# Optimization experiments

Measured on AMD Instinct MI355X. Metric: run time of the kernel, lower is better.

## Reference

```python
import jax, jax.numpy as jnp
import numpy as np

N = 50000      # nodes
E = 800000     # edges (avg degree 16)
H = 128        # hidden_dim
F_IN = 128     # node_in_dim
EPS = 1e-8     # torch cosine_similarity eps
ALPHA = 0.3


def _xavier(k, shape):
    fan_out, fan_in = shape
    lim = float(np.sqrt(6.0 / (fan_in + fan_out)))
    return jax.random.uniform(k, shape, minval=-lim, maxval=lim, dtype=jnp.float32)


PARAM_SHAPES = [
    ("w_lq", (H, 1)), ("w_lf", (H, F_IN)),
    ("wq0", (H, 1)), ("wq1", (H, H)), ("wq2", (H, H)),
    ("wx0", (H, F_IN)), ("wx1", (H, H)), ("wx2", (H, H)),
    ("wf0", (H, H)), ("wf1", (H, H)), ("wf2", (H, H)),
    ("m1_w1", (H, H)), ("m1_w2", (H, H)),
    ("m2_w1", (1, H)), ("m2_w2", (1, 1)),
]
BIAS_OF = {"w_lq": "b_lq", "w_lf": "b_lf", "wq0": "bq0", "wq1": "bq1", "wq2": "bq2",
           "wx0": "bx0", "wx1": "bx1", "wx2": "bx2", "wf0": "bf0", "wf1": "bf1",
           "wf2": "bf2", "m1_w1": "m1_b1", "m1_w2": "m1_b2", "m2_w1": "m2_b1", "m2_w2": "m2_b2"}


def setup_inputs() -> dict:
    key = jax.random.key(0)
    ks = jax.random.split(key, 3 + len(PARAM_SHAPES))
    inp = {
        "q": 42,
        "feats": jax.random.normal(ks[0], (N, F_IN), dtype=jnp.float32),
        "edge_index": jax.random.randint(ks[1], (2, E), 0, N, dtype=jnp.int64),
        "neg_edge_index": jax.random.randint(ks[2], (2, E), 0, N, dtype=jnp.int64),
    }
    for i, (name, shape) in enumerate(PARAM_SHAPES):
        inp[name] = _xavier(ks[3 + i], shape)
        inp[BIAS_OF[name]] = jnp.zeros((shape[0],), jnp.float32)
    return inp


def _forward(q, feats, edge_index, neg_edge_index,
             w_lq, b_lq, w_lf, b_lf,
             wq0, bq0, wq1, bq1, wq2, bq2,
             wx0, bx0, wx1, bx1, wx2, bx2,
             wf0, bf0, wf1, bf1, wf2, bf2,
             m1_w1, m1_b1, m1_w2, m1_b2,
             m2_w1, m2_b1, m2_w2, m2_b2):
    n = feats.shape[0]
    src, dst = edge_index[0], edge_index[1]

    # GCN symmetric normalization with self-loops (edge_weight = 1)
    deg = jax.ops.segment_sum(jnp.ones(src.shape[0], feats.dtype), dst, num_segments=n) + 1.0
    dis = deg ** -0.5
    norm_e = dis[src] * dis[dst]        # per-edge norm
    inv_deg = 1.0 / deg                 # self-loop norm d^-1/2 * d^-1/2

    def lin(x, W, b):
        return x @ W.T + b

    def gcn(x, W, b):
        xw = x @ W.T                                                      # [n,H]
        agg = jax.ops.segment_sum(xw[src] * norm_e[:, None], dst, num_segments=n)
        return agg + xw * inv_deg[:, None] + b

    querys = jnp.zeros((n, 1), feats.dtype).at[q, 0].set(1.0)
    querys_ = lin(querys, w_lq, b_lq)
    feats_ = lin(feats, w_lf, b_lf)

    # layer 0
    hq = jax.nn.relu(gcn(querys, wq0, bq0))
    h = jax.nn.relu(gcn(feats, wx0, bx0))
    hf = jax.nn.relu(hq + h + gcn(querys_ + feats_, wf0, bf0))
    # middle layer (num_layers - 2 == 1 iteration, eval mode: dropout identity)
    hq = jax.nn.relu(gcn(hq, wq1, bq1))
    h = jax.nn.relu(gcn(h, wx1, bx1))
    hf = jax.nn.relu(hq + h + gcn(hf, wf1, bf1))
    # final layer (no relu)
    hq = gcn(hq, wq2, bq2)
    h = gcn(h, wx2, bx2)
    hf = hq + h + gcn(hf, wf2, bf2)

    x = lin(jax.nn.relu(lin(hf, m1_w1, m1_b1)), m1_w2, m1_b2)  # mlp1

    # ---- decode (attack_type != 'proposed') ----
    q_emb = x[q]
    qn = jnp.maximum(jnp.linalg.norm(q_emb), EPS)

    def cos_q(v):  # cosine similarity of rows of v with q_emb (torch eps semantics)
        vn = jnp.maximum(jnp.linalg.norm(v, axis=-1), EPS)
        return (v @ q_emb) / (vn * qn)

    # reconstruct loss: BCE-with-logits on cosine edge scores
    pos_s = cos_q((x[src] + x[dst]) * 0.5)
    neg_s = cos_q((x[neg_edge_index[0]] + x[neg_edge_index[1]]) * 0.5)
    loss_recon = jnp.mean(jax.nn.softplus(-pos_s)) + jnp.mean(jax.nn.softplus(neg_s))

    sim_xq = cos_q(x)                                            # [n]
    sim_xx = lin(jax.nn.relu(lin(x, m2_w1, m2_b1)), m2_w2, m2_b2)[:, 0]  # mlp2
    sim = ((1.0 - ALPHA) * sim_xq + ALPHA * sim_xx) * 2.0
    return jax.nn.sigmoid(sim), loss_recon


def reference(q, feats, edge_index, neg_edge_index,
              w_lq, b_lq, w_lf, b_lf,
              wq0, bq0, wq1, bq1, wq2, bq2,
              wx0, bx0, wx1, bx1, wx2, bx2,
              wf0, bf0, wf1, bf1, wf2, bf2,
              m1_w1, m1_b1, m1_w2, m1_b2,
              m2_w1, m2_b1, m2_w2, m2_b2):
    return _forward(q, feats, edge_index, neg_edge_index,
                    w_lq, b_lq, w_lf, b_lf,
                    wq0, bq0, wq1, bq1, wq2, bq2,
                    wx0, bx0, wx1, bx1, wx2, bx2,
                    wf0, bf0, wf1, bf1, wf2, bf2,
                    m1_w1, m1_b1, m1_w2, m1_b2,
                    m2_w1, m2_b1, m2_w2, m2_b2)
```

## Files before the change

kernel.cpp:

```cpp
#include <hip/hip_runtime.h>
#include <math.h>

#define N_NODES 50000
#define N_EDGES 800000
#define EPSV 1e-8f
#define ALPHA 0.3f

typedef __attribute__((ext_vector_type(8))) unsigned short ushort8;
typedef __attribute__((ext_vector_type(4))) float floatx4;
typedef __attribute__((ext_vector_type(2))) long longx2;
typedef _Float16 half8 __attribute__((ext_vector_type(8)));
typedef _Float16 half2v __attribute__((ext_vector_type(2)));

__device__ inline unsigned short f2h(float f) {
    union { _Float16 h; unsigned short u; } c; c.h = (_Float16)f; return c.u;
}
__device__ inline float h2f(unsigned short u) {
    union { unsigned short u; _Float16 h; } c; c.u = u; return (float)c.h;
}
__device__ inline unsigned char f2e4m3(float f) {
    unsigned u = __float_as_uint(f);
    unsigned s = (u >> 24) & 0x80u;
    float af = fabsf(f);
    if (af >= 464.f) return (unsigned char)(s | 0x7Eu);
    if (af < 0.015625f) {
        int m = (int)rintf(af * 512.f);
        return (unsigned char)(s | (unsigned)m);
    }
    unsigned au = __float_as_uint(af);
    unsigned mant = au & 0x7FFFFFu;
    unsigned lsb = (mant >> 20) & 1u;
    mant += 0x7FFFFu + lsb;
    unsigned exp32 = (au >> 23) + (mant >> 23);
    mant &= 0x7FFFFFu;
    unsigned e8 = exp32 - 127u + 7u;
    return (unsigned char)(s | (e8 << 3) | (mant >> 20));
}
__device__ inline int qperm(int k) {
    return ((k >> 3) & 3) * 32 + (k >> 5) * 8 + (k & 7);
}


__global__ __launch_bounds__(256) void k_count(const int* __restrict__ ei,
                                               int* __restrict__ cnt) {
    int e = blockIdx.x * 256 + threadIdx.x;
    if (e < N_EDGES) atomicAdd(&cnt[__builtin_nontemporal_load(ei + N_EDGES + e)], 1);
}

__global__ __launch_bounds__(256) void k_invdis(const int* __restrict__ cnt,
                                                float* __restrict__ dis,
                                                float* __restrict__ inv) {
    int i = blockIdx.x * 256 + threadIdx.x;
    if (i < N_NODES) {
        float d = (float)cnt[i] + 1.0f;
        dis[i] = 1.0f / sqrtf(d);
        inv[i] = 1.0f / d;
    }
}

__global__ __launch_bounds__(256) void k_scan_partial(const int* __restrict__ cnt,
                                                      int* __restrict__ partial) {
    int b = blockIdx.x, t = threadIdx.x;
    int base = b * 1024 + t * 4;
    int s = 0;
#pragma unroll
    for (int j = 0; j < 4; ++j) {
        int idx = base + j;
        if (idx < N_NODES) s += cnt[idx];
    }
#pragma unroll
    for (int m = 1; m < 64; m <<= 1) s += __shfl_xor(s, m, 64);
    __shared__ int sh[4];
    if ((t & 63) == 0) sh[t >> 6] = s;
    __syncthreads();
    if (t == 0) partial[b] = sh[0] + sh[1] + sh[2] + sh[3];
}

__global__ void k_scan_mid(int* __restrict__ partial, int* __restrict__ rowptr) {
    int l = threadIdx.x;
    const int NP = (N_NODES + 1023) / 1024;
    int v = (l < NP) ? partial[l] : 0;
    int vin = v;
#pragma unroll
    for (int off = 1; off < 64; off <<= 1) {
        int u = __shfl_up(v, off, 64);
        if (l >= off) v += u;
    }
    if (l < NP) partial[l] = v - vin;
    if (l == NP - 1) rowptr[N_NODES] = v;
}

__global__ __launch_bounds__(256) void k_scan_final(const int* __restrict__ cnt,
                                                    const int* __restrict__ partial,
                                                    int* __restrict__ rowptr) {
    int b = blockIdx.x, t = threadIdx.x;
    int base = b * 1024 + t * 4;
    int c[4];
    int s = 0;
#pragma unroll
    for (int j = 0; j < 4; ++j) {
        int idx = base + j;
        c[j] = (idx < N_NODES) ? cnt[idx] : 0;
        s += c[j];
    }
    __shared__ int sh[256];
    sh[t] = s;
    __syncthreads();
    for (int off = 1; off < 256; off <<= 1) {
        int v = 0;
        if (t >= off) v = sh[t - off];
        __syncthreads();
        sh[t] += v;
        __syncthreads();
    }
    int texcl = sh[t] - s;
    int pre = partial[b] + texcl;
#pragma unroll
    for (int j = 0; j < 4; ++j) {
        int idx = base + j;
        if (idx < N_NODES) rowptr[idx] = pre;
        pre += c[j];
    }
}

__global__ __launch_bounds__(256) void k_fill(const int* __restrict__ ei,
                                              const int* __restrict__ rowptr,
                                              int* __restrict__ cursor,
                                              int* __restrict__ col) {
    int e = blockIdx.x * 256 + threadIdx.x;
    if (e < N_EDGES) {
        int d = __builtin_nontemporal_load(ei + N_EDGES + e);
        int pos = rowptr[d] + atomicAdd(&cursor[d], 1);
        col[pos] = __builtin_nontemporal_load(ei + e);
    }
}

__global__ __launch_bounds__(256) void k_t(const int* __restrict__ ei,
                                           const int* __restrict__ qp,
                                           const float* __restrict__ dis,
                                           const float* __restrict__ inv,
                                           float* __restrict__ t) {
    int e = blockIdx.x * 256 + threadIdx.x;
    int q = *qp;
    if (e == 0) atomicAdd(&t[q], inv[q]);
    if (e < N_EDGES && __builtin_nontemporal_load(ei + e) == q) {
        int d = ei[N_EDGES + e];
        atomicAdd(&t[d], dis[q] * dis[d]);
    }
}

__global__ void k_rank1(const float* __restrict__ bq0, const float* __restrict__ bq1,
                        const float* __restrict__ wq0, const float* __restrict__ wq1,
                        const float* __restrict__ wq2, int* __restrict__ flag,
                        float* __restrict__ r0v, float* __restrict__ r1v,
                        float* __restrict__ g2v) {
    int j = threadIdx.x;
    unsigned long long b = __ballot(bq0[j] != 0.f || bq1[j] != 0.f);
    __shared__ int bad[2];
    __shared__ float r0s[128], r1s[128];
    if ((j & 63) == 0) bad[j >> 6] = (b != 0ull);
    __syncthreads();
    int fl = !(bad[0] | bad[1]);
    if (j == 0) flag[0] = fl;
    if (!fl) return;
    float r0 = fmaxf(wq0[j], 0.f);
    r0s[j] = r0;
    r0v[j] = r0;
    __syncthreads();
    float s = 0.f;
    for (int k = 0; k < 128; k += 4) {
        float4 w = *(const float4*)(wq1 + j * 128 + k);
        s += w.x * r0s[k] + w.y * r0s[k + 1] + w.z * r0s[k + 2] + w.w * r0s[k + 3];
    }
    float r1 = fmaxf(s, 0.f);
    r1s[j] = r1;
    r1v[j] = r1;
    __syncthreads();
    float s2 = 0.f;
    for (int k = 0; k < 128; k += 4) {
        float4 w = *(const float4*)(wq2 + j * 128 + k);
        s2 += w.x * r1s[k] + w.y * r1s[k + 1] + w.z * r1s[k + 2] + w.w * r1s[k + 3];
    }
    g2v[j] = s2;
}

__global__ __launch_bounds__(256) void k_spmv(const int* __restrict__ gflag,
                                              const int* __restrict__ rowptr,
                                              const int* __restrict__ col,
                                              const float* __restrict__ dis,
                                              const float* __restrict__ inv,
                                              const float* __restrict__ vin,
                                              float* __restrict__ vout) {
    if (*gflag != 1) return;
    int i = blockIdx.x * 256 + threadIdx.x;
    if (i >= N_NODES) return;
    int r0 = rowptr[i], r1 = rowptr[i + 1];
    float s = 0.f;
    for (int e = r0; e < r1; ++e) {
        int c = col[e];
        s += dis[c] * vin[c];
    }
    vout[i] = fmaf(inv[i], vin[i], dis[i] * s);
}

__global__ __launch_bounds__(256) void k_cast(const float* __restrict__ in,
                                              unsigned short* __restrict__ out, int n8) {
    int id = blockIdx.x * 256 + threadIdx.x;
    if (id >= n8) return;
    const float4 a = *(const float4*)(in + id * 8);
    const float4 b = *(const float4*)(in + id * 8 + 4);
    ushort8 o;
    o[0] = f2h(a.x); o[1] = f2h(a.y); o[2] = f2h(a.z); o[3] = f2h(a.w);
    o[4] = f2h(b.x); o[5] = f2h(b.y); o[6] = f2h(b.z); o[7] = f2h(b.w);
    *(ushort8*)(out + id * 8) = o;
}

struct WPack { const float* w[11]; };
__global__ __launch_bounds__(256) void k_castw(WPack wp, unsigned short* __restrict__ out) {
    int m = blockIdx.y;
    int id = blockIdx.x * 256 + threadIdx.x;
    const float* src = wp.w[m] + id * 8;
    float4 a = *(const float4*)src;
    float4 b = *(const float4*)(src + 4);
    ushort8 o;
    o[0] = f2h(a.x); o[1] = f2h(a.y); o[2] = f2h(a.z); o[3] = f2h(a.w);
    o[4] = f2h(b.x); o[5] = f2h(b.y); o[6] = f2h(b.z); o[7] = f2h(b.w);
    *(ushort8*)(out + m * 16384 + id * 8) = o;
}


__device__ __forceinline__ void gemm_core(
    const unsigned short* __restrict__ A, int As,
    const unsigned short* __restrict__ Wb, int nrows, int row0,
    unsigned short* Al, unsigned short* Wl, floatx4 (&acc)[8][2]) {
    const int tid = threadIdx.x;
    const int wv = tid >> 6;
    const int t4 = tid >> 4, c16 = tid & 15;

#pragma unroll
    for (int it = 0; it < 8; ++it) {
        int r = it * 16 + t4;
        int gr = row0 + r; if (gr > nrows - 1) gr = nrows - 1;
        int sw = (c16 * 16) ^ ((r & 7) << 4);
        const char* srcA = (const char*)(A + (size_t)gr * As) + sw;
        __builtin_amdgcn_global_load_lds(
            (const __attribute__((address_space(1))) void*)srcA,
            (__attribute__((address_space(3))) void*)(Al + it * 2048 + wv * 512),
            16, 0, 0);
        const char* srcW = (const char*)(Wb + r * 128) + sw;
        __builtin_amdgcn_global_load_lds(
            (const __attribute__((address_space(1))) void*)srcW,
            (__attribute__((address_space(3))) void*)(Wl + it * 2048 + wv * 512),
            16, 0, 0);
    }
    __syncthreads();

    const int l = tid & 63;
    const int lr = l & 15, lg = l >> 4;
    const int sx = (lr & 7) << 4;

#pragma unroll
    for (int i = 0; i < 8; ++i)
#pragma unroll
        for (int j = 0; j < 2; ++j) acc[i][j] = (floatx4){0.f, 0.f, 0.f, 0.f};

#pragma unroll
    for (int ks = 0; ks < 4; ++ks) {
        int ko = (ks * 64 + lg * 16) ^ sx;
        half8 bfr[2];
#pragma unroll
        for (int ct = 0; ct < 2; ++ct) {
            int c = wv * 32 + ct * 16 + lr;
            bfr[ct] = *(const half8*)((char*)Wl + c * 256 + ko);
        }
#pragma unroll
        for (int rt = 0; rt < 8; ++rt) {
            int r = rt * 16 + lr;
            half8 af = *(const half8*)((char*)Al + r * 256 + ko);
            acc[rt][0] = __builtin_amdgcn_mfma_f32_16x16x32_f16(af, bfr[0], acc[rt][0], 0, 0, 0);
            acc[rt][1] = __builtin_amdgcn_mfma_f32_16x16x32_f16(af, bfr[1], acc[rt][1], 0, 0, 0);
        }
    }
}

template <int RELU, int HASB2, int WOUT>
__global__ __launch_bounds__(256) void k_gemm(
    const unsigned short* __restrict__ A, int As,
    const unsigned short* __restrict__ Wb,
    const float* __restrict__ bias, const float* __restrict__ bias2,
    const int* __restrict__ gflag, int want,
    unsigned short* __restrict__ outh, int ohs,
    float* __restrict__ outf, unsigned char* __restrict__ outq, int nrows) {
    if (gflag && *gflag != want) return;
    __shared__ unsigned short Al[128 * 128];
    __shared__ unsigned short Wl[128 * 128];
    const int row0 = blockIdx.x * 128;
    floatx4 acc[8][2];
    gemm_core(A, As, Wb, nrows, row0, Al, Wl, acc);

    const int l = threadIdx.x & 63, wv = threadIdx.x >> 6;
    const int lr = l & 15, lg = l >> 4;
#pragma unroll
    for (int ct = 0; ct < 2; ++ct) {
        int colc = wv * 32 + ct * 16 + lr;
        float bv = bias[colc];
        if (HASB2) bv += bias2[colc];
        int qp_ = WOUT == 2 ? qperm(colc) : 0;
#pragma unroll
        for (int rt = 0; rt < 8; ++rt) {
            int rbase = row0 + rt * 16 + lg * 4;
#pragma unroll
            for (int reg = 0; reg < 4; ++reg) {
                int r = rbase + reg;
                if (r >= nrows) continue;
                float v = acc[rt][ct][reg] + bv;
                if (RELU) v = fmaxf(v, 0.f);
                if (WOUT == 2) {
                    outf[(size_t)r * 128 + colc] = v;
                    outq[(size_t)r * 128 + qp_] = f2e4m3(v);
                } else {
                    outh[(size_t)r * ohs + colc] = f2h(v);
                }
            }
        }
    }
}

template <int RELU>
__global__ __launch_bounds__(256) void k_gemmF(
    const unsigned short* __restrict__ A, int As,
    const unsigned short* __restrict__ Wb,
    const float* __restrict__ bias, const float* __restrict__ bias2,
    const unsigned short* __restrict__ addh, int ahs,
    const unsigned short* __restrict__ addhq, int aqs,
    const float* __restrict__ u, const float* __restrict__ vq,
    const int* __restrict__ gflag,
    unsigned short* __restrict__ outh, int ohs, int nrows) {
    __shared__ unsigned short Al[128 * 128];
    __shared__ unsigned short Wl[128 * 128];
    const int row0 = blockIdx.x * 128;
    floatx4 acc[8][2];
    gemm_core(A, As, Wb, nrows, row0, Al, Wl, acc);

    const int fl = *gflag;
    const int l = threadIdx.x & 63, wv = threadIdx.x >> 6;
    const int lr = l & 15, lg = l >> 4;
#pragma unroll
    for (int ct = 0; ct < 2; ++ct) {
        int colc = wv * 32 + ct * 16 + lr;
        float bv = bias[colc];
        float vqc = 0.f;
        if (fl) {
            vqc = vq[colc];
            if (bias2) bv += bias2[colc];
        }
#pragma unroll
        for (int rt = 0; rt < 8; ++rt) {
            int rbase = row0 + rt * 16 + lg * 4;
#pragma unroll
            for (int reg = 0; reg < 4; ++reg) {
                int r = rbase + reg;
                if (r >= nrows) continue;
                float v = acc[rt][ct][reg] + bv;
                if (fl) v = fmaf(u[r], vqc, v);
                else v += h2f(addhq[(size_t)r * aqs + colc]);
                v += h2f(addh[(size_t)r * ahs + colc]);
                if (RELU) v = fmaxf(v, 0.f);
                outh[(size_t)r * ohs + colc] = f2h(v);
            }
        }
    }
}


template <int NUM>
__device__ __forceinline__ void agg_body(
    const int* __restrict__ rowptr, const int* __restrict__ col,
    const float* __restrict__ dis, const float* __restrict__ inv,
    const unsigned short* __restrict__ in0, int s0,
    const unsigned short* __restrict__ in1, int s1,
    const unsigned short* __restrict__ in2, int s2,
    unsigned short* __restrict__ out, int o0, int o1, int o2) {
    int i = blockIdx.x * 4 + (threadIdx.x >> 6);
    int l = threadIdx.x & 63;
    int g = l >> 4, li = l & 15;
    int r0 = rowptr[i], r1 = rowptr[i + 1];

    half2v accA[NUM][4], accB[NUM][4];
#pragma unroll
    for (int b = 0; b < NUM; ++b)
#pragma unroll
        for (int j = 0; j < 4; ++j) {
            accA[b][j] = (half2v){(_Float16)0, (_Float16)0};
            accB[b][j] = (half2v){(_Float16)0, (_Float16)0};
        }

    union U8 { ushort8 u; half2v h[4]; };
    const unsigned short* ins[3] = {in0, in1, in2};
    const int ss[3] = {s0, s1, s2};

    for (int base = r0; base < r1; base += 8) {
        int eA = base + g, eB = base + 4 + g;
        int sA = i; float wA = 0.f;
        if (eA < r1) { sA = col[eA]; wA = dis[sA]; }
        int sB = i; float wB = 0.f;
        if (eB < r1) { sB = col[eB]; wB = dis[sB]; }
        _Float16 whA = (_Float16)wA, whB = (_Float16)wB;
        half2v w2A = {whA, whA}, w2B = {whB, whB};
        U8 vA[NUM], vB[NUM];
#pragma unroll
        for (int b = 0; b < NUM; ++b) {
            vA[b].u = *(const ushort8*)(ins[b] + (size_t)sA * ss[b] + li * 8);
            vB[b].u = *(const ushort8*)(ins[b] + (size_t)sB * ss[b] + li * 8);
        }
#pragma unroll
        for (int b = 0; b < NUM; ++b)
#pragma unroll
            for (int j = 0; j < 4; ++j) {
                accA[b][j] += vA[b].h[j] * w2A;
                accB[b][j] += vB[b].h[j] * w2B;
            }
    }
    union U2 { half2v h; int i; };
#pragma unroll
    for (int b = 0; b < NUM; ++b)
#pragma unroll
        for (int j = 0; j < 4; ++j) {
            U2 c, o;
            c.h = accA[b][j] + accB[b][j];
            o.i = __shfl_xor(c.i, 16, 64); c.h += o.h;
            o.i = __shfl_xor(c.i, 32, 64); c.h += o.h;
            accA[b][j] = c.h;
        }
    if (g == 0) {
        float di = dis[i], iv = inv[i];
        const int oo[3] = {o0, o1, o2};
#pragma unroll
        for (int b = 0; b < NUM; ++b) {
            U8 sv;
            sv.u = *(const ushort8*)(ins[b] + (size_t)i * ss[b] + li * 8);
            ushort8 o;
#pragma unroll
            for (int j = 0; j < 4; ++j) {
                float a0 = fmaf(di, (float)accA[b][j][0], iv * (float)sv.h[j][0]);
                float a1 = fmaf(di, (float)accA[b][j][1], iv * (float)sv.h[j][1]);
                o[2 * j] = f2h(a0);
                o[2 * j + 1] = f2h(a1);
            }
            *(ushort8*)(out + (size_t)i * 384 + oo[b] + li * 8) = o;
        }
    }
}

__global__ __launch_bounds__(256) void k_agg0(
    const int* __restrict__ rowptr, const int* __restrict__ col,
    const float* __restrict__ dis, const float* __restrict__ inv,
    const unsigned short* __restrict__ featsh, const unsigned short* __restrict__ z0h,
    unsigned short* __restrict__ out) {
    agg_body<2>(rowptr, col, dis, inv, featsh, 128, z0h, 128, nullptr, 0,
                out, 128, 256, 0);
}

__global__ __launch_bounds__(256) void k_aggL(
    const int* __restrict__ gflag,
    const int* __restrict__ rowptr, const int* __restrict__ col,
    const float* __restrict__ dis, const float* __restrict__ inv,
    const unsigned short* __restrict__ B1h, unsigned short* __restrict__ B2h) {
    if (*gflag == 1)
        agg_body<2>(rowptr, col, dis, inv, B1h + 128, 384, B1h + 256, 384,
                    nullptr, 0, B2h, 128, 256, 0);
    else
        agg_body<3>(rowptr, col, dis, inv, B1h, 384, B1h + 128, 384,
                    B1h + 256, 384, B2h, 0, 128, 256);
}

__global__ __launch_bounds__(256) void k_hq0(const int* __restrict__ gflag,
                                             const float* __restrict__ t,
                                             const float* __restrict__ wq0,
                                             const float* __restrict__ bq0,
                                             unsigned short* __restrict__ B1h) {
    if (*gflag != 0) return;
    int gidx = blockIdx.x * 256 + threadIdx.x;
    int i = gidx >> 7, j = gidx & 127;
    B1h[(size_t)i * 384 + j] = f2h(fmaxf(fmaf(t[i], wq0[j], bq0[j]), 0.f));
}

__global__ void k_addwlq(const int* __restrict__ qp, const float* __restrict__ w_lq,
                         unsigned short* __restrict__ z0h) {
    int j = threadIdx.x;
    int q = *qp;
    z0h[(size_t)q * 128 + j] = f2h(h2f(z0h[(size_t)q * 128 + j]) + w_lq[j]);
}


__global__ void k_qemb(const int* __restrict__ qp, const float* __restrict__ xf,
                       float* __restrict__ qe) {
    int j = threadIdx.x;
    int q = *qp;
    float v = xf[(size_t)q * 128 + j];
    qe[j] = v;
    float s = v * v;
#pragma unroll
    for (int m = 1; m < 64; m <<= 1) s += __shfl_xor(s, m, 64);
    __shared__ float sh[2];
    if ((j & 63) == 0) sh[j >> 6] = s;
    __syncthreads();
    if (j == 0) qe[128] = fmaxf(sqrtf(sh[0] + sh[1]), EPSV);
}

__global__ __launch_bounds__(256) void k_node(const float* __restrict__ xf,
                                              const float* __restrict__ qe,
                                              const float* __restrict__ m2w1,
                                              const float* __restrict__ m2b1,
                                              const float* __restrict__ m2w2,
                                              const float* __restrict__ m2b2,
                                              float* __restrict__ out,
                                              float* __restrict__ a,
                                              float* __restrict__ n2) {
    int node = blockIdx.x * 4 + (threadIdx.x >> 6);
    int lane = threadIdx.x & 63;
    const float2 xv = *(const float2*)(xf + (size_t)node * 128 + 2 * lane);
    const float2 qv = *(const float2*)(qe + 2 * lane);
    const float2 wv = *(const float2*)(m2w1 + 2 * lane);
    float dq = xv.x * qv.x + xv.y * qv.y;
    float dx = xv.x * xv.x + xv.y * xv.y;
    float dw = xv.x * wv.x + xv.y * wv.y;
#pragma unroll
    for (int m = 1; m < 64; m <<= 1) {
        dq += __shfl_xor(dq, m, 64);
        dx += __shfl_xor(dx, m, 64);
        dw += __shfl_xor(dw, m, 64);
    }
    if (lane == 0) {
        float qn = qe[128];
        float vn = fmaxf(sqrtf(dx), EPSV);
        float simq = dq / (vn * qn);
        float l1 = dw + m2b1[0];
        float s2 = fmaxf(l1, 0.f) * m2w2[0] + m2b2[0];
        float sim = ((1.f - ALPHA) * simq + ALPHA * s2) * 2.f;
        out[node] = 1.f / (1.f + expf(-sim));
        a[node] = dq;
        n2[node] = dx;
    }
}

__global__ __launch_bounds__(256) void k_loss(const int* __restrict__ ei,
                                              const int* __restrict__ nei,
                                              const unsigned char* __restrict__ xq8,
                                              const float* __restrict__ a,
                                              const float* __restrict__ n2,
                                              const float* __restrict__ qe,
                                              float* __restrict__ lossout) {
    int l = threadIdx.x & 63, wvi = threadIdx.x >> 6;
    int i16 = l & 15;
    int kb = l >> 4;
    int gw = blockIdx.x * 4 + wvi;
    const int NW = gridDim.x * 4;
    const int NT = 2 * N_EDGES / 16;
    float qn = qe[128];
    float local = 0.f;
    const int rsel = l & 3;
    const int srcl = ((i16 >> 2) << 4) + i16;

    int t = gw;
    for (; t + 3 * NW < NT; t += 4 * NW) {
        int s[4], d[4], neg[4];
        longx2 a01[4], a23[4], b01[4], b23[4];
        float n2s[4], n2d[4], as_[4], ad_[4];
#pragma unroll
        for (int p_ = 0; p_ < 4; ++p_) {
            int base = (t + p_ * NW) * 16;
            neg[p_] = base >= N_EDGES;
            const int* Ep = neg[p_] ? nei : ei;
            int eo = neg[p_] ? base - N_EDGES : base;
            s[p_] = __builtin_nontemporal_load(Ep + eo + i16);
            d[p_] = __builtin_nontemporal_load(Ep + eo + i16 + N_EDGES);
        }
#pragma unroll
        for (int p_ = 0; p_ < 4; ++p_) {
            const unsigned char* ps = xq8 + (size_t)s[p_] * 128 + kb * 32;
            const unsigned char* pd = xq8 + (size_t)d[p_] * 128 + kb * 32;
            a01[p_] = *(const longx2*)ps;
            a23[p_] = *(const longx2*)(ps + 16);
            b01[p_] = *(const longx2*)pd;
            b23[p_] = *(const longx2*)(pd + 16);
            n2s[p_] = 0.f; n2d[p_] = 0.f; as_[p_] = 0.f; ad_[p_] = 0.f;
            if (l < 16) {
                n2s[p_] = n2[s[p_]]; n2d[p_] = n2[d[p_]];
                as_[p_] = a[s[p_]]; ad_[p_] = a[d[p_]];
            }
        }
#pragma unroll
        for (int p_ = 0; p_ < 4; ++p_) {
            floatx4 acc = (floatx4){0.f, 0.f, 0.f, 0.f};
            acc = __builtin_amdgcn_mfma_f32_16x16x32_fp8_fp8(a01[p_][0], b01[p_][0], acc, 0, 0, 0);
            acc = __builtin_amdgcn_mfma_f32_16x16x32_fp8_fp8(a01[p_][1], b01[p_][1], acc, 0, 0, 0);
            acc = __builtin_amdgcn_mfma_f32_16x16x32_fp8_fp8(a23[p_][0], b23[p_][0], acc, 0, 0, 0);
            acc = __builtin_amdgcn_mfma_f32_16x16x32_fp8_fp8(a23[p_][1], b23[p_][1], acc, 0, 0, 0);
            float v = acc[0];
            v = (rsel == 1) ? acc[1] : v;
            v = (rsel == 2) ? acc[2] : v;
            v = (rsel == 3) ? acc[3] : v;
            float dsd = __int_as_float(
                __builtin_amdgcn_ds_bpermute(srcl << 2, __float_as_int(v)));
            if (l < 16) {
                float nv = 0.25f * (n2s[p_] + n2d[p_] + 2.f * dsd);
                float vn = fmaxf(sqrtf(fmaxf(nv, 0.f)), EPSV);
                float cs = (0.5f * (as_[p_] + ad_[p_])) / (vn * qn);
                float sg = neg[p_] ? cs : -cs;
                local += log1pf(expf(sg));
            }
        }
    }
    for (; t < NT; t += NW) {
        int base = t * 16;
        int neg = base >= N_EDGES;
        const int* Ep = neg ? nei : ei;
        int eo = neg ? base - N_EDGES : base;
        int s = Ep[eo + i16], d = Ep[eo + i16 + N_EDGES];
        const unsigned char* ps = xq8 + (size_t)s * 128 + kb * 32;
        const unsigned char* pd = xq8 + (size_t)d * 128 + kb * 32;
        longx2 a01 = *(const longx2*)ps;
        longx2 a23 = *(const longx2*)(ps + 16);
        longx2 b01 = *(const longx2*)pd;
        longx2 b23 = *(const longx2*)(pd + 16);
        floatx4 acc = (floatx4){0.f, 0.f, 0.f, 0.f};
        acc = __builtin_amdgcn_mfma_f32_16x16x32_fp8_fp8(a01[0], b01[0], acc, 0, 0, 0);
        acc = __builtin_amdgcn_mfma_f32_16x16x32_fp8_fp8(a01[1], b01[1], acc, 0, 0, 0);
        acc = __builtin_amdgcn_mfma_f32_16x16x32_fp8_fp8(a23[0], b23[0], acc, 0, 0, 0);
        acc = __builtin_amdgcn_mfma_f32_16x16x32_fp8_fp8(a23[1], b23[1], acc, 0, 0, 0);
        float v = acc[0];
        v = (rsel == 1) ? acc[1] : v;
        v = (rsel == 2) ? acc[2] : v;
        v = (rsel == 3) ? acc[3] : v;
        float dsd = __int_as_float(
            __builtin_amdgcn_ds_bpermute(srcl << 2, __float_as_int(v)));
        if (l < 16) {
            float nv = 0.25f * (n2[s] + n2[d] + 2.f * dsd);
            float vn = fmaxf(sqrtf(fmaxf(nv, 0.f)), EPSV);
            float cs = (0.5f * (a[s] + a[d])) / (vn * qn);
            float sg = neg ? cs : -cs;
            local += log1pf(expf(sg));
        }
    }
    local += __shfl_xor(local, 1, 64);
    local += __shfl_xor(local, 2, 64);
    local += __shfl_xor(local, 4, 64);
    local += __shfl_xor(local, 8, 64);
    __shared__ float sh[4];
    if (l == 0) sh[wvi] = local;
    __syncthreads();
    if (threadIdx.x == 0)
        atomicAdd(lossout, (sh[0] + sh[1] + sh[2] + sh[3]) * (1.f / N_EDGES));
}


extern "C" void kernel_launch(void* const* d_in, const int* in_sizes, int n_in,
                              void* d_out, int out_size, void* d_ws, size_t ws_size,
                              hipStream_t stream) {
    const int* qp = (const int*)d_in[0];
    const float* feats = (const float*)d_in[1];
    const int* ei = (const int*)d_in[2];
    const int* nei = (const int*)d_in[3];
    const float *w_lq = (const float*)d_in[4], *b_lq = (const float*)d_in[5];
    const float *w_lf = (const float*)d_in[6], *b_lf = (const float*)d_in[7];
    const float *wq0 = (const float*)d_in[8], *bq0 = (const float*)d_in[9];
    const float *wq1 = (const float*)d_in[10], *bq1 = (const float*)d_in[11];
    const float *wq2 = (const float*)d_in[12], *bq2 = (const float*)d_in[13];
    const float *wx0 = (const float*)d_in[14], *bx0 = (const float*)d_in[15];
    const float *wx1 = (const float*)d_in[16], *bx1 = (const float*)d_in[17];
    const float *wx2 = (const float*)d_in[18], *bx2 = (const float*)d_in[19];
    const float *wf0 = (const float*)d_in[20], *bf0 = (const float*)d_in[21];
    const float *wf1 = (const float*)d_in[22], *bf1 = (const float*)d_in[23];
    const float *wf2 = (const float*)d_in[24], *bf2 = (const float*)d_in[25];
    const float *m1w1 = (const float*)d_in[26], *m1b1 = (const float*)d_in[27];
    const float *m1w2 = (const float*)d_in[28], *m1b2 = (const float*)d_in[29];
    const float *m2w1 = (const float*)d_in[30], *m2b1 = (const float*)d_in[31];
    const float *m2w2 = (const float*)d_in[32], *m2b2 = (const float*)d_in[33];
    float* out = (float*)d_out;

    char* p = (char*)d_ws;
    auto alloc = [&](size_t b) -> char* {
        char* r = p;
        p += (b + 255) & ~(size_t)255;
        return r;
    };
    float* dis = (float*)alloc(N_NODES * 4);
    float* inv = (float*)alloc(N_NODES * 4);
    float* t = (float*)alloc(N_NODES * 4);
    float* qe = (float*)alloc(129 * 4);
    float* a = (float*)alloc(N_NODES * 4);
    float* n2 = (float*)alloc(N_NODES * 4);
    float* u1 = (float*)alloc(N_NODES * 4);
    float* u2 = (float*)alloc(N_NODES * 4);
    float* r0v = (float*)alloc(128 * 4);
    float* r1v = (float*)alloc(128 * 4);
    float* g2v = (float*)alloc(128 * 4);
    int* flag = (int*)alloc(4);
    int* cnt = (int*)alloc(N_NODES * 4);
    int* cursor = (int*)alloc(N_NODES * 4);
    int* rowptr = (int*)alloc((N_NODES + 1) * 4);
    int* partial = (int*)alloc(64 * 4);
    int* col = (int*)alloc(N_EDGES * 4);
    unsigned short* Wb = (unsigned short*)alloc((size_t)11 * 16384 * 2);
    unsigned short* featsh = (unsigned short*)alloc((size_t)N_NODES * 128 * 2);
    unsigned short* z0h = (unsigned short*)alloc((size_t)N_NODES * 128 * 2);
    unsigned short* B1h = (unsigned short*)alloc((size_t)N_NODES * 384 * 2);
    unsigned short* B2h = (unsigned short*)alloc((size_t)N_NODES * 384 * 2);
    unsigned char* xq8 = (unsigned char*)alloc((size_t)N_NODES * 128);
    float* xf = (float*)alloc((size_t)N_NODES * 128 * 4);

    const int EB = (N_EDGES + 255) / 256;
    const int NB = (N_NODES + 255) / 256;
    const int NP = (N_NODES + 1023) / 1024;
    const int GB = (N_NODES + 127) / 128;

    hipMemsetAsync(cnt, 0, N_NODES * 4, stream);
    hipMemsetAsync(cursor, 0, N_NODES * 4, stream);
    hipMemsetAsync(t, 0, N_NODES * 4, stream);
    hipMemsetAsync(out + N_NODES, 0, 4, stream);

    k_count<<<EB, 256, 0, stream>>>(ei, cnt);
    k_invdis<<<NB, 256, 0, stream>>>(cnt, dis, inv);
    k_scan_partial<<<NP, 256, 0, stream>>>(cnt, partial);
    k_scan_mid<<<1, 64, 0, stream>>>(partial, rowptr);
    k_scan_final<<<NP, 256, 0, stream>>>(cnt, partial, rowptr);
    k_fill<<<EB, 256, 0, stream>>>(ei, rowptr, cursor, col);
    k_t<<<EB, 256, 0, stream>>>(ei, qp, dis, inv, t);
    k_rank1<<<1, 128, 0, stream>>>(bq0, bq1, wq0, wq1, wq2, flag, r0v, r1v, g2v);
    k_cast<<<(N_NODES * 128 / 8 + 255) / 256, 256, 0, stream>>>(feats, featsh,
                                                                N_NODES * 128 / 8);
    WPack wp{{w_lf, wx0, wf0, wq1, wx1, wf1, wq2, wx2, wf2, m1w1, m1w2}};
    k_castw<<<dim3(8, 11), 256, 0, stream>>>(wp, Wb);
    k_spmv<<<NB, 256, 0, stream>>>(flag, rowptr, col, dis, inv, t, u1);
    k_spmv<<<NB, 256, 0, stream>>>(flag, rowptr, col, dis, inv, u1, u2);

    k_gemm<0, 1, 0><<<GB, 256, 0, stream>>>(featsh, 128, Wb + 0 * 16384, b_lf, b_lq,
                                            nullptr, 0, z0h, 128, nullptr, nullptr, N_NODES);
    k_addwlq<<<1, 128, 0, stream>>>(qp, w_lq, z0h);

    k_hq0<<<(N_NODES * 128) / 256, 256, 0, stream>>>(flag, t, wq0, bq0, B1h);
    k_agg0<<<N_NODES / 4, 256, 0, stream>>>(rowptr, col, dis, inv, featsh, z0h, B2h);
    k_gemm<1, 0, 0><<<GB, 256, 0, stream>>>(B2h + 128, 384, Wb + 1 * 16384, bx0, nullptr,
                                            nullptr, 0, B1h + 128, 384, nullptr, nullptr, N_NODES);
    k_gemmF<1><<<GB, 256, 0, stream>>>(B2h + 256, 384, Wb + 2 * 16384, bf0, nullptr,
                                       B1h + 128, 384, B1h + 0, 384,
                                       t, r0v, flag, B1h + 256, 384, N_NODES);

    k_aggL<<<N_NODES / 4, 256, 0, stream>>>(flag, rowptr, col, dis, inv, B1h, B2h);
    k_gemm<1, 0, 0><<<GB, 256, 0, stream>>>(B2h + 0, 384, Wb + 3 * 16384, bq1, nullptr,
                                            flag, 0, B1h + 0, 384, nullptr, nullptr, N_NODES);
    k_gemm<1, 0, 0><<<GB, 256, 0, stream>>>(B2h + 128, 384, Wb + 4 * 16384, bx1, nullptr,
                                            nullptr, 0, B1h + 128, 384, nullptr, nullptr, N_NODES);
    k_gemmF<1><<<GB, 256, 0, stream>>>(B2h + 256, 384, Wb + 5 * 16384, bf1, nullptr,
                                       B1h + 128, 384, B1h + 0, 384,
                                       u1, r1v, flag, B1h + 256, 384, N_NODES);

    k_aggL<<<N_NODES / 4, 256, 0, stream>>>(flag, rowptr, col, dis, inv, B1h, B2h);
    k_gemm<0, 0, 0><<<GB, 256, 0, stream>>>(B2h + 0, 384, Wb + 6 * 16384, bq2, nullptr,
                                            flag, 0, B1h + 0, 384, nullptr, nullptr, N_NODES);
    k_gemm<0, 0, 0><<<GB, 256, 0, stream>>>(B2h + 128, 384, Wb + 7 * 16384, bx2, nullptr,
                                            nullptr, 0, B1h + 128, 384, nullptr, nullptr, N_NODES);
    k_gemmF<0><<<GB, 256, 0, stream>>>(B2h + 256, 384, Wb + 8 * 16384, bf2, bq2,
                                       B1h + 128, 384, B1h + 0, 384,
                                       u2, g2v, flag, B1h + 256, 384, N_NODES);

    k_gemm<1, 0, 0><<<GB, 256, 0, stream>>>(B1h + 256, 384, Wb + 9 * 16384, m1b1, nullptr,
                                            nullptr, 0, B2h + 0, 384, nullptr, nullptr, N_NODES);
    k_gemm<0, 0, 2><<<GB, 256, 0, stream>>>(B2h + 0, 384, Wb + 10 * 16384, m1b2, nullptr,
                                            nullptr, 0, nullptr, 0, xf, xq8, N_NODES);

    k_qemb<<<1, 128, 0, stream>>>(qp, xf, qe);
    k_node<<<N_NODES / 4, 256, 0, stream>>>(xf, qe, m2w1, m2b1, m2w2, m2b2, out, a, n2);
    k_loss<<<2048, 256, 0, stream>>>(ei, nei, xq8, a, n2, qe, out + N_NODES);
}
```

Baseline: 643.5 us.

## Parallelize rank-1 matvecs, split aggregation kernels, retune gather and loss unrolling

Splits the single-block rank-1 chain into a flag kernel plus two 128-block wavefront matvec kernels, so the serial per-thread dot products over wq1 and wq2 run in parallel. Splits the flag-branching aggregation into two kernels that each exit early depending on the flag, which avoids instantiating both template paths in one kernel and may lower register pressure, at the cost of an extra launch. Widens the edge gather loop to 16 neighbours per iteration for more loads in flight. Reduces loss-kernel unrolling from 4 to 2 and doubles its grid, trading per-wave memory parallelism for occupancy.

```diff
diff --git a/kernel.cpp b/kernel.cpp
--- a/kernel.cpp
+++ b/kernel.cpp
@@ -149,39 +149,29 @@
     }
 }
 
-__global__ void k_rank1(const float* __restrict__ bq0, const float* __restrict__ bq1,
-                        const float* __restrict__ wq0, const float* __restrict__ wq1,
-                        const float* __restrict__ wq2, int* __restrict__ flag,
-                        float* __restrict__ r0v, float* __restrict__ r1v,
-                        float* __restrict__ g2v) {
+__global__ void k_flagr0(const float* __restrict__ bq0, const float* __restrict__ bq1,
+                         const float* __restrict__ wq0, int* __restrict__ flag,
+                         float* __restrict__ r0v) {
     int j = threadIdx.x;
     unsigned long long b = __ballot(bq0[j] != 0.f || bq1[j] != 0.f);
     __shared__ int bad[2];
-    __shared__ float r0s[128], r1s[128];
     if ((j & 63) == 0) bad[j >> 6] = (b != 0ull);
     __syncthreads();
-    int fl = !(bad[0] | bad[1]);
-    if (j == 0) flag[0] = fl;
-    if (!fl) return;
-    float r0 = fmaxf(wq0[j], 0.f);
-    r0s[j] = r0;
-    r0v[j] = r0;
-    __syncthreads();
-    float s = 0.f;
-    for (int k = 0; k < 128; k += 4) {
-        float4 w = *(const float4*)(wq1 + j * 128 + k);
-        s += w.x * r0s[k] + w.y * r0s[k + 1] + w.z * r0s[k + 2] + w.w * r0s[k + 3];
-    }
-    float r1 = fmaxf(s, 0.f);
-    r1s[j] = r1;
-    r1v[j] = r1;
-    __syncthreads();
-    float s2 = 0.f;
-    for (int k = 0; k < 128; k += 4) {
-        float4 w = *(const float4*)(wq2 + j * 128 + k);
-        s2 += w.x * r1s[k] + w.y * r1s[k + 1] + w.z * r1s[k + 2] + w.w * r1s[k + 3];
-    }
-    g2v[j] = s2;
+    if (j == 0) flag[0] = !(bad[0] | bad[1]);
+    r0v[j] = fmaxf(wq0[j], 0.f);
+}
+
+template <int RELU>
+__global__ void k_matvec(const int* __restrict__ gflag, const float* __restrict__ W,
+                         const float* __restrict__ vin, float* __restrict__ vout) {
+    if (*gflag != 1) return;
+    int c = blockIdx.x, l = threadIdx.x;
+    float2 w = *(const float2*)(W + c * 128 + 2 * l);
+    float2 v = *(const float2*)(vin + 2 * l);
+    float s = w.x * v.x + w.y * v.y;
+#pragma unroll
+    for (int m = 1; m < 64; m <<= 1) s += __shfl_xor(s, m, 64);
+    if (l == 0) vout[c] = RELU ? fmaxf(s, 0.f) : s;
 }
 
 __global__ __launch_bounds__(256) void k_spmv(const int* __restrict__ gflag,
@@ -399,19 +389,25 @@
     const unsigned short* ins[3] = {in0, in1, in2};
     const int ss[3] = {s0, s1, s2};
 
-    for (int base = r0; base < r1; base += 8) {
-        int eA = base + g, eB = base + 4 + g;
-        int sA = i; float wA = 0.f;
+    for (int base = r0; base < r1; base += 16) {
+        int eA = base + g, eB = base + 4 + g, eC = base + 8 + g, eD = base + 12 + g;
+        int sA = i, sB = i, sC = i, sD = i;
+        float wA = 0.f, wB = 0.f, wC = 0.f, wD = 0.f;
         if (eA < r1) { sA = col[eA]; wA = dis[sA]; }
-        int sB = i; float wB = 0.f;
         if (eB < r1) { sB = col[eB]; wB = dis[sB]; }
+        if (eC < r1) { sC = col[eC]; wC = dis[sC]; }
+        if (eD < r1) { sD = col[eD]; wD = dis[sD]; }
         _Float16 whA = (_Float16)wA, whB = (_Float16)wB;
+        _Float16 whC = (_Float16)wC, whD = (_Float16)wD;
         half2v w2A = {whA, whA}, w2B = {whB, whB};
-        U8 vA[NUM], vB[NUM];
+        half2v w2C = {whC, whC}, w2D = {whD, whD};
+        U8 vA[NUM], vB[NUM], vC[NUM], vD[NUM];
 #pragma unroll
         for (int b = 0; b < NUM; ++b) {
             vA[b].u = *(const ushort8*)(ins[b] + (size_t)sA * ss[b] + li * 8);
             vB[b].u = *(const ushort8*)(ins[b] + (size_t)sB * ss[b] + li * 8);
+            vC[b].u = *(const ushort8*)(ins[b] + (size_t)sC * ss[b] + li * 8);
+            vD[b].u = *(const ushort8*)(ins[b] + (size_t)sD * ss[b] + li * 8);
         }
 #pragma unroll
         for (int b = 0; b < NUM; ++b)
@@ -419,6 +415,8 @@
             for (int j = 0; j < 4; ++j) {
                 accA[b][j] += vA[b].h[j] * w2A;
                 accB[b][j] += vB[b].h[j] * w2B;
+                accA[b][j] += vC[b].h[j] * w2C;
+                accB[b][j] += vD[b].h[j] * w2D;
             }
     }
     union U2 { half2v h; int i; };
@@ -461,17 +459,24 @@
                 out, 128, 256, 0);
 }
 
-__global__ __launch_bounds__(256) void k_aggL(
+__global__ __launch_bounds__(256) void k_agg3(
     const int* __restrict__ gflag,
     const int* __restrict__ rowptr, const int* __restrict__ col,
     const float* __restrict__ dis, const float* __restrict__ inv,
     const unsigned short* __restrict__ B1h, unsigned short* __restrict__ B2h) {
-    if (*gflag == 1)
-        agg_body<2>(rowptr, col, dis, inv, B1h + 128, 384, B1h + 256, 384,
-                    nullptr, 0, B2h, 128, 256, 0);
-    else
-        agg_body<3>(rowptr, col, dis, inv, B1h, 384, B1h + 128, 384,
-                    B1h + 256, 384, B2h, 0, 128, 256);
+    if (*gflag != 0) return;
+    agg_body<3>(rowptr, col, dis, inv, B1h, 384, B1h + 128, 384,
+                B1h + 256, 384, B2h, 0, 128, 256);
+}
+
+__global__ __launch_bounds__(256) void k_agg2(
+    const int* __restrict__ gflag,
+    const int* __restrict__ rowptr, const int* __restrict__ col,
+    const float* __restrict__ dis, const float* __restrict__ inv,
+    const unsigned short* __restrict__ B1h, unsigned short* __restrict__ B2h) {
+    if (*gflag != 1) return;
+    agg_body<2>(rowptr, col, dis, inv, B1h + 128, 384, B1h + 256, 384,
+                nullptr, 0, B2h, 128, 256, 0);
 }
 
 __global__ __launch_bounds__(256) void k_hq0(const int* __restrict__ gflag,
@@ -563,40 +568,48 @@
     const int srcl = ((i16 >> 2) << 4) + i16;
 
     int t = gw;
-    for (; t + 3 * NW < NT; t += 4 * NW) {
-        int s[4], d[4], neg[4];
-        longx2 a01[4], a23[4], b01[4], b23[4];
-        float n2s[4], n2d[4], as_[4], ad_[4];
-#pragma unroll
-        for (int p_ = 0; p_ < 4; ++p_) {
-            int base = (t + p_ * NW) * 16;
-            neg[p_] = base >= N_EDGES;
-            const int* Ep = neg[p_] ? nei : ei;
-            int eo = neg[p_] ? base - N_EDGES : base;
-            s[p_] = __builtin_nontemporal_load(Ep + eo + i16);
-            d[p_] = __builtin_nontemporal_load(Ep + eo + i16 + N_EDGES);
-        }
-#pragma unroll
-        for (int p_ = 0; p_ < 4; ++p_) {
-            const unsigned char* ps = xq8 + (size_t)s[p_] * 128 + kb * 32;
-            const unsigned char* pd = xq8 + (size_t)d[p_] * 128 + kb * 32;
-            a01[p_] = *(const longx2*)ps;
-            a23[p_] = *(const longx2*)(ps + 16);
-            b01[p_] = *(const longx2*)pd;
-            b23[p_] = *(const longx2*)(pd + 16);
-            n2s[p_] = 0.f; n2d[p_] = 0.f; as_[p_] = 0.f; ad_[p_] = 0.f;
-            if (l < 16) {
-                n2s[p_] = n2[s[p_]]; n2d[p_] = n2[d[p_]];
-                as_[p_] = a[s[p_]]; ad_[p_] = a[d[p_]];
-            }
-        }
-#pragma unroll
-        for (int p_ = 0; p_ < 4; ++p_) {
+    for (; t + NW < NT; t += 2 * NW) {
+        int baseA = t * 16;
+        int negA = baseA >= N_EDGES;
+        const int* EpA = negA ? nei : ei;
+        int eoA = negA ? baseA - N_EDGES : baseA;
+        int sA = __builtin_nontemporal_load(EpA + eoA + i16);
+        int dA = __builtin_nontemporal_load(EpA + eoA + i16 + N_EDGES);
+
+        int baseB = (t + NW) * 16;
+        int negB = baseB >= N_EDGES;
+        const int* EpB = negB ? nei : ei;
+        int eoB = negB ? baseB - N_EDGES : baseB;
+        int sB = __builtin_nontemporal_load(EpB + eoB + i16);
+        int dB = __builtin_nontemporal_load(EpB + eoB + i16 + N_EDGES);
+
+        const unsigned char* psA = xq8 + (size_t)sA * 128 + kb * 32;
+        const unsigned char* pdA = xq8 + (size_t)dA * 128 + kb * 32;
+        longx2 a01A = *(const longx2*)psA;
+        longx2 a23A = *(const longx2*)(psA + 16);
+        longx2 b01A = *(const longx2*)pdA;
+        longx2 b23A = *(const longx2*)(pdA + 16);
+
+        const unsigned char* psB = xq8 + (size_t)sB * 128 + kb * 32;
+        const unsigned char* pdB = xq8 + (size_t)dB * 128 + kb * 32;
+        longx2 a01B = *(const longx2*)psB;
+        longx2 a23B = *(const longx2*)(psB + 16);
+        longx2 b01B = *(const longx2*)pdB;
+        longx2 b23B = *(const longx2*)(pdB + 16);
+
+        float n2sA = 0.f, n2dA = 0.f, asA = 0.f, adA = 0.f;
+        float n2sB = 0.f, n2dB = 0.f, asB = 0.f, adB = 0.f;
+        if (l < 16) {
+            n2sA = n2[sA]; n2dA = n2[dA]; asA = a[sA]; adA = a[dA];
+            n2sB = n2[sB]; n2dB = n2[dB]; asB = a[sB]; adB = a[dB];
+        }
+
+        {
             floatx4 acc = (floatx4){0.f, 0.f, 0.f, 0.f};
-            acc = __builtin_amdgcn_mfma_f32_16x16x32_fp8_fp8(a01[p_][0], b01[p_][0], acc, 0, 0, 0);
-            acc = __builtin_amdgcn_mfma_f32_16x16x32_fp8_fp8(a01[p_][1], b01[p_][1], acc, 0, 0, 0);
-            acc = __builtin_amdgcn_mfma_f32_16x16x32_fp8_fp8(a23[p_][0], b23[p_][0], acc, 0, 0, 0);
-            acc = __builtin_amdgcn_mfma_f32_16x16x32_fp8_fp8(a23[p_][1], b23[p_][1], acc, 0, 0, 0);
+            acc = __builtin_amdgcn_mfma_f32_16x16x32_fp8_fp8(a01A[0], b01A[0], acc, 0, 0, 0);
+            acc = __builtin_amdgcn_mfma_f32_16x16x32_fp8_fp8(a01A[1], b01A[1], acc, 0, 0, 0);
+            acc = __builtin_amdgcn_mfma_f32_16x16x32_fp8_fp8(a23A[0], b23A[0], acc, 0, 0, 0);
+            acc = __builtin_amdgcn_mfma_f32_16x16x32_fp8_fp8(a23A[1], b23A[1], acc, 0, 0, 0);
             float v = acc[0];
             v = (rsel == 1) ? acc[1] : v;
             v = (rsel == 2) ? acc[2] : v;
@@ -604,15 +617,35 @@
             float dsd = __int_as_float(
                 __builtin_amdgcn_ds_bpermute(srcl << 2, __float_as_int(v)));
             if (l < 16) {
-                float nv = 0.25f * (n2s[p_] + n2d[p_] + 2.f * dsd);
+                float nv = 0.25f * (n2sA + n2dA + 2.f * dsd);
                 float vn = fmaxf(sqrtf(fmaxf(nv, 0.f)), EPSV);
-                float cs = (0.5f * (as_[p_] + ad_[p_])) / (vn * qn);
-                float sg = neg[p_] ? cs : -cs;
+                float cs = (0.5f * (asA + adA)) / (vn * qn);
+                float sg = negA ? cs : -cs;
                 local += log1pf(expf(sg));
             }
         }
-    }
-    for (; t < NT; t += NW) {
+        {
+            floatx4 acc = (floatx4){0.f, 0.f, 0.f, 0.f};
+            acc = __builtin_amdgcn_mfma_f32_16x16x32_fp8_fp8(a01B[0], b01B[0], acc, 0, 0, 0);
+            acc = __builtin_amdgcn_mfma_f32_16x16x32_fp8_fp8(a01B[1], b01B[1], acc, 0, 0, 0);
+            acc = __builtin_amdgcn_mfma_f32_16x16x32_fp8_fp8(a23B[0], b23B[0], acc, 0, 0, 0);
+            acc = __builtin_amdgcn_mfma_f32_16x16x32_fp8_fp8(a23B[1], b23B[1], acc, 0, 0, 0);
+            float v = acc[0];
+            v = (rsel == 1) ? acc[1] : v;
+            v = (rsel == 2) ? acc[2] : v;
+            v = (rsel == 3) ? acc[3] : v;
+            float dsd = __int_as_float(
+                __builtin_amdgcn_ds_bpermute(srcl << 2, __float_as_int(v)));
+            if (l < 16) {
+                float nv = 0.25f * (n2sB + n2dB + 2.f * dsd);
+                float vn = fmaxf(sqrtf(fmaxf(nv, 0.f)), EPSV);
+                float cs = (0.5f * (asB + adB)) / (vn * qn);
+                float sg = negB ? cs : -cs;
+                local += log1pf(expf(sg));
+            }
+        }
+    }
+    if (t < NT) {
         int base = t * 16;
         int neg = base >= N_EDGES;
         const int* Ep = neg ? nei : ei;
@@ -727,11 +760,13 @@
     k_scan_final<<<NP, 256, 0, stream>>>(cnt, partial, rowptr);
     k_fill<<<EB, 256, 0, stream>>>(ei, rowptr, cursor, col);
     k_t<<<EB, 256, 0, stream>>>(ei, qp, dis, inv, t);
-    k_rank1<<<1, 128, 0, stream>>>(bq0, bq1, wq0, wq1, wq2, flag, r0v, r1v, g2v);
+    k_flagr0<<<1, 128, 0, stream>>>(bq0, bq1, wq0, flag, r0v);
     k_cast<<<(N_NODES * 128 / 8 + 255) / 256, 256, 0, stream>>>(feats, featsh,
                                                                 N_NODES * 128 / 8);
     WPack wp{{w_lf, wx0, wf0, wq1, wx1, wf1, wq2, wx2, wf2, m1w1, m1w2}};
     k_castw<<<dim3(8, 11), 256, 0, stream>>>(wp, Wb);
+    k_matvec<1><<<128, 64, 0, stream>>>(flag, wq1, r0v, r1v);
+    k_matvec<0><<<128, 64, 0, stream>>>(flag, wq2, r1v, g2v);
     k_spmv<<<NB, 256, 0, stream>>>(flag, rowptr, col, dis, inv, t, u1);
     k_spmv<<<NB, 256, 0, stream>>>(flag, rowptr, col, dis, inv, u1, u2);
 
@@ -747,7 +782,8 @@
                                        B1h + 128, 384, B1h + 0, 384,
                                        t, r0v, flag, B1h + 256, 384, N_NODES);
 
-    k_aggL<<<N_NODES / 4, 256, 0, stream>>>(flag, rowptr, col, dis, inv, B1h, B2h);
+    k_agg3<<<N_NODES / 4, 256, 0, stream>>>(flag, rowptr, col, dis, inv, B1h, B2h);
+    k_agg2<<<N_NODES / 4, 256, 0, stream>>>(flag, rowptr, col, dis, inv, B1h, B2h);
     k_gemm<1, 0, 0><<<GB, 256, 0, stream>>>(B2h + 0, 384, Wb + 3 * 16384, bq1, nullptr,
                                             flag, 0, B1h + 0, 384, nullptr, nullptr, N_NODES);
     k_gemm<1, 0, 0><<<GB, 256, 0, stream>>>(B2h + 128, 384, Wb + 4 * 16384, bx1, nullptr,
@@ -756,7 +792,8 @@
                                        B1h + 128, 384, B1h + 0, 384,
                                        u1, r1v, flag, B1h + 256, 384, N_NODES);
 
-    k_aggL<<<N_NODES / 4, 256, 0, stream>>>(flag, rowptr, col, dis, inv, B1h, B2h);
+    k_agg3<<<N_NODES / 4, 256, 0, stream>>>(flag, rowptr, col, dis, inv, B1h, B2h);
+    k_agg2<<<N_NODES / 4, 256, 0, stream>>>(flag, rowptr, col, dis, inv, B1h, B2h);
     k_gemm<0, 0, 0><<<GB, 256, 0, stream>>>(B2h + 0, 384, Wb + 6 * 16384, bq2, nullptr,
                                             flag, 0, B1h + 0, 384, nullptr, nullptr, N_NODES);
     k_gemm<0, 0, 0><<<GB, 256, 0, stream>>>(B2h + 128, 384, Wb + 7 * 16384, bx2, nullptr,
@@ -772,5 +809,5 @@
 
     k_qemb<<<1, 128, 0, stream>>>(qp, xf, qe);
     k_node<<<N_NODES / 4, 256, 0, stream>>>(xf, qe, m2w1, m2b1, m2w2, m2b2, out, a, n2);
-    k_loss<<<2048, 256, 0, stream>>>(ei, nei, xq8, a, n2, qe, out + N_NODES);
-}
+    k_loss<<<4096, 256, 0, stream>>>(ei, nei, xq8, a, n2, qe, out + N_NODES);
+}
```

Measured after the change: 654.2 us. No clear change (+1.7%).
